# Optimization experiments

Measured on AMD Instinct MI355X. Metric: run time of the kernel, lower is better.

The kernel has to match this reference:

```python
import jax, jax.numpy as jnp
import numpy as np

N = 4096
FEAT = 5
H = 128
L = 3
K = 4
HD = H // K  # 32


def setup_inputs() -> dict:
    key = jax.random.key(0)
    ks = jax.random.split(key, 24)
    node_features = jax.random.normal(ks[0], (N, FEAT), dtype=jnp.float32)
    u = jax.random.uniform(ks[1], (N, N), dtype=jnp.float32)
    adj = jnp.where(u < 0.01, u, 0.0)
    adj = adj / (adj.sum(axis=1, keepdims=True) + 1e-8)  # row-normalised
    mask = jax.random.randint(ks[2], (N,), 0, 2).astype(bool)
    s = 0.05
    return {
        'node_features': node_features,
        'adj': adj,
        'mask': mask,
        'Wi': jax.random.normal(ks[3], (FEAT, H), jnp.float32) * s,
        'bi': jnp.zeros((H,), jnp.float32),
        'gat_W': jax.random.normal(ks[4], (L, K, H, HD), jnp.float32) * s,
        'gat_a': jax.random.normal(ks[5], (L, K, 2 * HD), jnp.float32) * s,
        'ln_g': jnp.ones((L, H), jnp.float32),
        'ln_b': jnp.zeros((L, H), jnp.float32),
        'pW1': jax.random.normal(ks[6], (H, H // 2), jnp.float32) * s,
        'pb1': jnp.zeros((H // 2,), jnp.float32),
        'pW2': jax.random.normal(ks[7], (H // 2, 1), jnp.float32) * s,
        'pb2': jnp.zeros((1,), jnp.float32),
        'poolW': jax.random.normal(ks[8], (H, H), jnp.float32) * s,
        'poolb': jnp.zeros((H,), jnp.float32),
        'poolv': jax.random.normal(ks[9], (H,), jnp.float32) * s,
        'vW1': jax.random.normal(ks[10], (H, H // 2), jnp.float32) * s,
        'vb1': jnp.zeros((H // 2,), jnp.float32),
        'vW2': jax.random.normal(ks[11], (H // 2, 1), jnp.float32) * s,
        'vb2': jnp.zeros((1,), jnp.float32),
    }


def _layernorm(x, g, b, eps=1e-5):
    mu = x.mean(-1, keepdims=True)
    var = ((x - mu) ** 2).mean(-1, keepdims=True)
    return (x - mu) / jnp.sqrt(var + eps) * g + b


def reference(node_features, adj, mask, Wi, bi, gat_W, gat_a, ln_g, ln_b,
              pW1, pb1, pW2, pb2, poolW, poolb, poolv, vW1, vb1, vW2, vb2):
    n = node_features.shape[0]
    x = jax.nn.relu(node_features @ Wi + bi)  # (N, H)
    edge_mask = (adj > 0) | jnp.eye(n, dtype=bool)  # (N, N) incl self-loops
    n_layers = gat_W.shape[0]
    for l in range(n_layers):
        Wx = jnp.einsum('nd,kdh->knh', x, gat_W[l])  # (K, N, hd)
        a_src = jnp.einsum('knh,kh->kn', Wx, gat_a[l][:, :HD])  # (K, N)
        a_dst = jnp.einsum('knh,kh->kn', Wx, gat_a[l][:, HD:])  # (K, N)
        e = jax.nn.leaky_relu(a_src[:, :, None] + a_dst[:, None, :], 0.2)  # (K,N,N)
        e = jnp.where(edge_mask[None], e, -jnp.inf)
        alpha = jax.nn.softmax(e, axis=-1)  # softmax over neighbours j
        h = jax.nn.elu(jnp.einsum('kij,kjh->kih', alpha, Wx))  # (K, N, hd)
        out = jnp.transpose(h, (1, 0, 2)).reshape(n, -1)  # concat heads -> (N, H)
        out = out + x  # residual (Identity: in_dim == out_dim)
        x = _layernorm(out, ln_g[l], ln_b[l])
    # policy head
    logits = (jax.nn.relu(x @ pW1 + pb1) @ pW2 + pb2).squeeze(-1)  # (N,)
    logits = jnp.where(mask, logits, -jnp.inf)
    # attention pooling restricted to masked (valid) nodes
    scores = jnp.tanh(x @ poolW + poolb) @ poolv  # (N,)
    scores = jnp.where(mask, scores, -jnp.inf)
    beta = jax.nn.softmax(scores)
    pooled = (beta[:, None] * x).sum(0)  # (H,)
    value = (jax.nn.relu(pooled @ vW1 + vb1) @ vW2 + vb2).squeeze(-1)  # scalar
    return logits, value
```

## Files before the change

kernel.cpp:

```cpp
#include <hip/hip_runtime.h>

#define NN 4096
#define FEAT 5
#define H 128
#define HD 32
#define KH 4
#define NEG_INF (-__builtin_inff())
#define MASK_SENTINEL (-1e30f)

#define WS_FLAG  0
#define WS_DEG   256
#define WS_NBR   (WS_DEG + NN*4)
#define WS_X     (WS_NBR + NN*128*2)
#define WS_WX    (WS_X + NN*H*4)
#define WS_ATS   (WS_WX + KH*NN*HD*4)
#define WS_ATD   (WS_ATS + NN*16)
#define WS_PART  (WS_ATD + NN*16)
#define WS_ZPART (WS_PART + 256*H*4)

__device__ __forceinline__ float red64(float v) {
#pragma unroll
    for (int off = 32; off; off >>= 1) v += __shfl_xor(v, off, 64);
    return v;
}
__device__ __forceinline__ float red64max(float v) {
#pragma unroll
    for (int off = 32; off; off >>= 1) v = fmaxf(v, __shfl_xor(v, off, 64));
    return v;
}
__device__ __forceinline__ float red32(float v) {
#pragma unroll
    for (int off = 16; off; off >>= 1) v += __shfl_xor(v, off, 32);
    return v;
}
__device__ __forceinline__ bool read_mask(const void* mp, int f, int n) {
    if (f == 3) return ((const long long*)mp)[n] != 0;
    if (f == 1) return ((const int*)mp)[n] != 0;
    if (f == 2) return ((const float*)mp)[n] != 0.f;
    return ((const unsigned char*)mp)[n] != 0;
}

__global__ __launch_bounds__(256) void k_csr_proj(
    const float* __restrict__ adj, const float* __restrict__ nf,
    const float* __restrict__ Wi, const float* __restrict__ bi,
    const void* mask, int* flag, int* __restrict__ deg,
    unsigned short* __restrict__ nbr, float* __restrict__ xbuf) {
    __shared__ int ln[4][128];
    int w = threadIdx.x >> 6, lane = threadIdx.x & 63;
    int row = blockIdx.x * 4 + w;
    ln[w][lane] = 0; ln[w][64 + lane] = 0;
    const float4* arow = (const float4*)(adj + (size_t)row * NN);
    int cnt = 0;
    bool self = false;
    for (int c0 = 0; c0 < NN / 4; c0 += 64) {
        float4 v = arow[c0 + lane];
        int cb = (c0 + lane) * 4;
        float vals[4] = {v.x, v.y, v.z, v.w};
#pragma unroll
        for (int s = 0; s < 4; s++) {
            bool nz = vals[s] > 0.f;
            if (nz && cb + s == row) self = true;
            unsigned long long b = __ballot((int)nz);
            if (nz) {
                int pos = cnt + __popcll(b & ((1ull << lane) - 1ull));
                if (pos < 128) ln[w][pos] = cb + s;
            }
            cnt += __popcll(b);
        }
    }
    bool anyself = __any((int)self);
    if (!anyself) {
        if (lane == 0 && cnt < 128) ln[w][cnt] = row;
        cnt++;
    }
    int d = cnt < 128 ? cnt : 128;
    if (lane == 0) deg[row] = d;
    nbr[(size_t)row * 128 + lane] = (unsigned short)ln[w][lane];
    nbr[(size_t)row * 128 + 64 + lane] = (unsigned short)ln[w][64 + lane];
    float a1 = bi[lane], a2 = bi[64 + lane];
#pragma unroll
    for (int f = 0; f < FEAT; f++) {
        float xv = nf[row * FEAT + f];
        a1 += xv * Wi[f * H + lane];
        a2 += xv * Wi[f * H + 64 + lane];
    }
    xbuf[(size_t)row * H + lane] = fmaxf(a1, 0.f);
    xbuf[(size_t)row * H + 64 + lane] = fmaxf(a2, 0.f);
    if (blockIdx.x == 0 && w == 0) {
        const unsigned* ip = (const unsigned*)mask;
        const float* fp = (const float*)mask;
        bool i32ok = true, i64ok = true, f32ok = true;
        for (int i = lane; i < 1024; i += 64) {
            unsigned v = ip[i];
            if (v > 1u) i32ok = false;
            if (i & 1) { if (v != 0u) i64ok = false; }
            else       { if (v > 1u) i64ok = false; }
            float fv = fp[i];
            if (fv != 0.f && fv != 1.f) f32ok = false;
        }
        i32ok = (__ballot((int)i32ok) == ~0ull);
        i64ok = (__ballot((int)i64ok) == ~0ull);
        f32ok = (__ballot((int)f32ok) == ~0ull);
        if (lane == 0) *flag = i64ok ? 3 : (i32ok ? 1 : (f32ok ? 2 : 0));
    }
}

__global__ __launch_bounds__(256) void k_wx(
    const float* __restrict__ xbuf, const float* __restrict__ gw,
    const float* __restrict__ ga, float* __restrict__ Wx,
    float* __restrict__ attS, float* __restrict__ attD) {
    __shared__ float xs[8][H];
    int t = threadIdx.x;
    int k = t >> 6, lane = t & 63, dh = lane >> 5, h = lane & 31;
    int n0 = blockIdx.x * 8;
    ((float4*)xs)[t] = ((const float4*)(xbuf + (size_t)n0 * H))[t];
    __syncthreads();
    float acc[8] = {0, 0, 0, 0, 0, 0, 0, 0};
    const float* g = gw + (size_t)k * (H * HD) + h;
    for (int dd = 0; dd < 64; dd += 4) {
        int d = dh * 64 + dd;
        float w0 = g[(size_t)(d + 0) * HD];
        float w1 = g[(size_t)(d + 1) * HD];
        float w2 = g[(size_t)(d + 2) * HD];
        float w3 = g[(size_t)(d + 3) * HD];
#pragma unroll
        for (int nn = 0; nn < 8; nn++) {
            float4 xv = *(const float4*)&xs[nn][d];
            acc[nn] += xv.x * w0 + xv.y * w1 + xv.z * w2 + xv.w * w3;
        }
    }
    float aws = ga[k * 64 + h], awd = ga[k * 64 + 32 + h];
#pragma unroll
    for (int nn = 0; nn < 8; nn++) {
        float full = acc[nn] + __shfl_xor(acc[nn], 32, 64);
        float s = red32(full * aws);
        float dv = red32(full * awd);
        int n = n0 + nn;
        if (dh == 0) Wx[(size_t)k * NN * HD + (size_t)n * HD + h] = full;
        if (lane == 0) { attS[n * 4 + k] = s; attD[n * 4 + k] = dv; }
    }
}

__global__ __launch_bounds__(256) void k_agg(
    const int* __restrict__ degG, const unsigned short* __restrict__ nbrG,
    const float* __restrict__ Wx, const float4* __restrict__ attS4,
    const float4* __restrict__ attD4, const float* __restrict__ lng,
    const float* __restrict__ lnb, float* __restrict__ xbuf) {
    __shared__ int s_nbr[128];
    __shared__ float s_o[H];
    __shared__ float s_red[2], s_red2[2];
    int t = threadIdx.x, w = t >> 6, lane = t & 63;
    int node = blockIdx.x;
    int k = w;
    int h = lane & 31, q = lane >> 5;
    int d = degG[node];
    if (t < 128) s_nbr[t] = nbrG[(size_t)node * 128 + t];
    __syncthreads();
    float4 aSv = attS4[node];
    float ai = k == 0 ? aSv.x : k == 1 ? aSv.y : k == 2 ? aSv.z : aSv.w;
    float e0 = NEG_INF, e1 = NEG_INF;
    if (lane < d) {
        float4 dv4 = attD4[s_nbr[lane]];
        float dvv = k == 0 ? dv4.x : k == 1 ? dv4.y : k == 2 ? dv4.z : dv4.w;
        float v = ai + dvv;
        e0 = v > 0.f ? v : 0.2f * v;
    }
    if (64 + lane < d) {
        float4 dv4 = attD4[s_nbr[64 + lane]];
        float dvv = k == 0 ? dv4.x : k == 1 ? dv4.y : k == 2 ? dv4.z : dv4.w;
        float v = ai + dvv;
        e1 = v > 0.f ? v : 0.2f * v;
    }
    float m = red64max(fmaxf(e0, e1));
    float p0 = (lane < d) ? __expf(e0 - m) : 0.f;
    float p1 = (64 + lane < d) ? __expf(e1 - m) : 0.f;
    float inv = 1.f / red64(p0 + p1);
    float acc = 0.f;
    const float* wxk = Wx + (size_t)k * NN * HD + h;
    int jmax = (d + 1) >> 1;
#pragma unroll 4
    for (int j = 0; j < jmax; j++) {
        int c = 2 * j + q;
        int sc = s_nbr[c];
        float al = (c < 64) ? __shfl(p0, c, 64) : __shfl(p1, c - 64, 64);
        acc += al * wxk[(size_t)sc * HD];
    }
    acc += __shfl_xor(acc, 32, 64);
    if (lane < 32) {
        float tot = acc * inv;
        float hv = tot > 0.f ? tot : __expf(tot) - 1.f;
        int dim = k * 32 + h;
        s_o[dim] = hv + xbuf[(size_t)node * H + dim];
    }
    __syncthreads();
    float o = (t < 128) ? s_o[t] : 0.f;
    float ps = red64(o);
    if (lane == 0 && w < 2) s_red[w] = ps;
    __syncthreads();
    float mu = (s_red[0] + s_red[1]) * (1.f / H);
    float dv = o - mu;
    float vs = red64((t < 128) ? dv * dv : 0.f);
    if (lane == 0 && w < 2) s_red2[w] = vs;
    __syncthreads();
    if (t < 128) {
        float var = (s_red2[0] + s_red2[1]) * (1.f / H);
        float rstd = rsqrtf(var + 1e-5f);
        xbuf[(size_t)node * H + t] = dv * rstd * lng[t] + lnb[t];
    }
}

__global__ __launch_bounds__(256) void k_heads(
    const float* __restrict__ xbuf, const float* __restrict__ pW1,
    const float* __restrict__ pb1, const float* __restrict__ pW2,
    const float* __restrict__ pb2, const float* __restrict__ poolW,
    const float* __restrict__ poolb, const float* __restrict__ poolv,
    const void* mask, const int* __restrict__ flag, float* __restrict__ out,
    float* __restrict__ part, float* __restrict__ zpart) {
    __shared__ float lds_x[16][H];
    __shared__ float lds_part[4][H];
    __shared__ float lds_z[4];
    int t = threadIdx.x, w = t >> 6, lane = t & 63;
    int n0b = blockIdx.x * 16;
    for (int idx = t; idx < 16 * H; idx += 256)
        lds_x[idx >> 7][idx & 127] = xbuf[(size_t)(n0b + (idx >> 7)) * H + (idx & 127)];
    __syncthreads();
    int nb = n0b + w * 4;
    float accp[4] = {0, 0, 0, 0}, acs1[4] = {0, 0, 0, 0}, acs2[4] = {0, 0, 0, 0};
#pragma unroll 2
    for (int d = 0; d < H; d++) {
        float w1 = pW1[d * 64 + lane];
        float q1 = poolW[d * H + lane];
        float q2 = poolW[d * H + 64 + lane];
#pragma unroll
        for (int nn = 0; nn < 4; nn++) {
            float xv = lds_x[w * 4 + nn][d];
            accp[nn] += xv * w1;
            acs1[nn] += xv * q1;
            acs2[nn] += xv * q2;
        }
    }
    int flg = *flag;
    float T = fminf(red64(fabsf(poolv[lane]) + fabsf(poolv[64 + lane])), 30.f);
    float pb1v = pb1[lane], pw2v = pW2[lane], pb2v = pb2[0];
    float pob1 = poolb[lane], pob2 = poolb[64 + lane];
    float pov1 = poolv[lane], pov2 = poolv[64 + lane];
    float pp1 = 0.f, pp2 = 0.f, zacc = 0.f;
#pragma unroll
    for (int nn = 0; nn < 4; nn++) {
        int node = nb + nn;
        float hp = red64(fmaxf(accp[nn] + pb1v, 0.f) * pw2v);
        float sc = red64(tanhf(acs1[nn] + pob1) * pov1 + tanhf(acs2[nn] + pob2) * pov2);
        bool mk = read_mask(mask, flg, node);
        if (lane == 0) out[node] = mk ? (hp + pb2v) : MASK_SENTINEL;
        float wn = mk ? __expf(sc - T) : 0.f;
        pp1 += wn * lds_x[w * 4 + nn][lane];
        pp2 += wn * lds_x[w * 4 + nn][64 + lane];
        zacc += wn;
    }
    lds_part[w][lane] = pp1;
    lds_part[w][64 + lane] = pp2;
    if (lane == 0) lds_z[w] = zacc;
    __syncthreads();
    if (w == 0) {
        float s1 = lds_part[0][lane] + lds_part[1][lane] + lds_part[2][lane] + lds_part[3][lane];
        float s2 = lds_part[0][64 + lane] + lds_part[1][64 + lane] +
                   lds_part[2][64 + lane] + lds_part[3][64 + lane];
        part[blockIdx.x * H + lane] = s1;
        part[blockIdx.x * H + 64 + lane] = s2;
        if (lane == 0) zpart[blockIdx.x] = lds_z[0] + lds_z[1] + lds_z[2] + lds_z[3];
    }
}

__global__ __launch_bounds__(1024) void k_value(
    const float* __restrict__ part, const float* __restrict__ zpart,
    const float* __restrict__ vW1, const float* __restrict__ vb1,
    const float* __restrict__ vW2, const float* __restrict__ vb2,
    float* __restrict__ out) {
    __shared__ float segsum[8][H];
    __shared__ float zfin[256];
    __shared__ float pooled[H];
    int t = threadIdx.x;
    int dim = t & 127, seg = t >> 7;
    float s = 0.f;
#pragma unroll 8
    for (int b = seg * 32; b < seg * 32 + 32; b++) s += part[b * H + dim];
    segsum[seg][dim] = s;
    if (t < 256) zfin[t] = zpart[t];
    __syncthreads();
    if (t < 512) {
        int sg = t >> 7;
        segsum[sg][dim] += segsum[sg + 4][dim];
    }
    if (t >= 512 && t < 640) zfin[t - 512] += zfin[t - 512 + 128];
    __syncthreads();
    if (t < 256) {
        int sg = t >> 7;
        segsum[sg][dim] += segsum[sg + 2][dim];
    }
    if (t >= 512 && t < 576) zfin[t - 512] += zfin[t - 512 + 64];
    __syncthreads();
    if (t < 128) segsum[0][dim] += segsum[1][dim];
    if (t >= 512 && t < 544) zfin[t - 512] += zfin[t - 512 + 32];
    __syncthreads();
    if (t < 32) {
        float z = zfin[t];
#pragma unroll
        for (int off = 16; off; off >>= 1) z += __shfl_xor(z, off, 32);
        if (t == 0) zfin[0] = z;
    }
    __syncthreads();
    float Z = zfin[0];
    if (t < H) pooled[t] = segsum[0][t] / Z;
    __syncthreads();
    if (t < 64) {
        float acc = vb1[t];
#pragma unroll 4
        for (int d = 0; d < H; d++) acc += pooled[d] * vW1[d * 64 + t];
        float v = red64(fmaxf(acc, 0.f) * vW2[t]);
        if (t == 0) out[NN] = v + vb2[0];
    }
}

extern "C" void kernel_launch(void* const* d_in, const int* in_sizes, int n_in,
                              void* d_out, int out_size, void* d_ws, size_t ws_size,
                              hipStream_t stream) {
    const float* nf    = (const float*)d_in[0];
    const float* adj   = (const float*)d_in[1];
    const void*  mask  = d_in[2];
    const float* Wi    = (const float*)d_in[3];
    const float* bi    = (const float*)d_in[4];
    const float* gat_W = (const float*)d_in[5];
    const float* gat_a = (const float*)d_in[6];
    const float* ln_g  = (const float*)d_in[7];
    const float* ln_b  = (const float*)d_in[8];
    const float* pW1   = (const float*)d_in[9];
    const float* pb1   = (const float*)d_in[10];
    const float* pW2   = (const float*)d_in[11];
    const float* pb2   = (const float*)d_in[12];
    const float* poolW = (const float*)d_in[13];
    const float* poolb = (const float*)d_in[14];
    const float* poolv = (const float*)d_in[15];
    const float* vW1   = (const float*)d_in[16];
    const float* vb1   = (const float*)d_in[17];
    const float* vW2   = (const float*)d_in[18];
    const float* vb2   = (const float*)d_in[19];

    char* ws = (char*)d_ws;
    int*            flag = (int*)(ws + WS_FLAG);
    int*            deg  = (int*)(ws + WS_DEG);
    unsigned short* nbr  = (unsigned short*)(ws + WS_NBR);
    float* xbuf  = (float*)(ws + WS_X);
    float* Wx    = (float*)(ws + WS_WX);
    float* ats   = (float*)(ws + WS_ATS);
    float* atd   = (float*)(ws + WS_ATD);
    float* partb = (float*)(ws + WS_PART);
    float* zpart = (float*)(ws + WS_ZPART);
    float* out   = (float*)d_out;

    const size_t GWL = KH * H * HD;
    const size_t GAL = KH * 2 * HD;

    k_csr_proj<<<1024, 256, 0, stream>>>(adj, nf, Wi, bi, mask, flag, deg, nbr, xbuf);
    for (int l = 0; l < 3; l++) {
        k_wx<<<512, 256, 0, stream>>>(xbuf, gat_W + l * GWL, gat_a + l * GAL,
                                      Wx, ats, atd);
        k_agg<<<4096, 256, 0, stream>>>(deg, nbr, Wx, (const float4*)ats,
                                        (const float4*)atd, ln_g + l * H,
                                        ln_b + l * H, xbuf);
    }
    k_heads<<<256, 256, 0, stream>>>(xbuf, pW1, pb1, pW2, pb2, poolW, poolb, poolv,
                                     mask, flag, out, partb, zpart);
    k_value<<<1, 1024, 0, stream>>>(partb, zpart, vW1, vb1, vW2, vb2, out);
}
```

Baseline: 178.0 us.

## Store Wx node-major and aggregate one node per wavefront with all heads

Wx is now written node-major (N x 128) instead of head-major, so each neighbour's four-head feature row is one contiguous 512-byte segment. k_agg now processes four nodes per block, one wavefront each. Each wave computes the softmax for all four heads at once and stores the normalised alphas in shared memory. Each lane then gathers float2 features and does the ELU, residual and layernorm with wave reductions only, which removes the block-wide barriers and shared-memory layernorm. The cost is more registers per lane and unconditional loads for padded neighbour slots, which depends on the neighbour padding holding valid indices.

```diff
diff --git a/kernel.cpp b/kernel.cpp
--- a/kernel.cpp
+++ b/kernel.cpp
@@ -13,7 +13,7 @@
 #define WS_NBR   (WS_DEG + NN*4)
 #define WS_X     (WS_NBR + NN*128*2)
 #define WS_WX    (WS_X + NN*H*4)
-#define WS_ATS   (WS_WX + KH*NN*HD*4)
+#define WS_ATS   (WS_WX + NN*H*4)
 #define WS_ATD   (WS_ATS + NN*16)
 #define WS_PART  (WS_ATD + NN*16)
 #define WS_ZPART (WS_PART + 256*H*4)
@@ -136,77 +136,81 @@
         float s = red32(full * aws);
         float dv = red32(full * awd);
         int n = n0 + nn;
-        if (dh == 0) Wx[(size_t)k * NN * HD + (size_t)n * HD + h] = full;
+        if (dh == 0) Wx[(size_t)n * H + k * 32 + h] = full;
         if (lane == 0) { attS[n * 4 + k] = s; attD[n * 4 + k] = dv; }
     }
 }
 
 __global__ __launch_bounds__(256) void k_agg(
     const int* __restrict__ degG, const unsigned short* __restrict__ nbrG,
-    const float* __restrict__ Wx, const float4* __restrict__ attS4,
+    const float* __restrict__ Wxn, const float4* __restrict__ attS4,
     const float4* __restrict__ attD4, const float* __restrict__ lng,
     const float* __restrict__ lnb, float* __restrict__ xbuf) {
-    __shared__ int s_nbr[128];
-    __shared__ float s_o[H];
-    __shared__ float s_red[2], s_red2[2];
+    __shared__ int s_nbr[4][128];
+    __shared__ float s_al[4][128][4];
     int t = threadIdx.x, w = t >> 6, lane = t & 63;
-    int node = blockIdx.x;
-    int k = w;
-    int h = lane & 31, q = lane >> 5;
+    int node = blockIdx.x * 4 + w;
     int d = degG[node];
-    if (t < 128) s_nbr[t] = nbrG[(size_t)node * 128 + t];
-    __syncthreads();
-    float4 aSv = attS4[node];
-    float ai = k == 0 ? aSv.x : k == 1 ? aSv.y : k == 2 ? aSv.z : aSv.w;
-    float e0 = NEG_INF, e1 = NEG_INF;
-    if (lane < d) {
-        float4 dv4 = attD4[s_nbr[lane]];
-        float dvv = k == 0 ? dv4.x : k == 1 ? dv4.y : k == 2 ? dv4.z : dv4.w;
-        float v = ai + dvv;
-        e0 = v > 0.f ? v : 0.2f * v;
-    }
-    if (64 + lane < d) {
-        float4 dv4 = attD4[s_nbr[64 + lane]];
-        float dvv = k == 0 ? dv4.x : k == 1 ? dv4.y : k == 2 ? dv4.z : dv4.w;
-        float v = ai + dvv;
-        e1 = v > 0.f ? v : 0.2f * v;
-    }
-    float m = red64max(fmaxf(e0, e1));
-    float p0 = (lane < d) ? __expf(e0 - m) : 0.f;
-    float p1 = (64 + lane < d) ? __expf(e1 - m) : 0.f;
-    float inv = 1.f / red64(p0 + p1);
-    float acc = 0.f;
-    const float* wxk = Wx + (size_t)k * NN * HD + h;
-    int jmax = (d + 1) >> 1;
-#pragma unroll 4
-    for (int j = 0; j < jmax; j++) {
-        int c = 2 * j + q;
-        int sc = s_nbr[c];
-        float al = (c < 64) ? __shfl(p0, c, 64) : __shfl(p1, c - 64, 64);
-        acc += al * wxk[(size_t)sc * HD];
-    }
-    acc += __shfl_xor(acc, 32, 64);
-    if (lane < 32) {
-        float tot = acc * inv;
-        float hv = tot > 0.f ? tot : __expf(tot) - 1.f;
-        int dim = k * 32 + h;
-        s_o[dim] = hv + xbuf[(size_t)node * H + dim];
-    }
-    __syncthreads();
-    float o = (t < 128) ? s_o[t] : 0.f;
-    float ps = red64(o);
-    if (lane == 0 && w < 2) s_red[w] = ps;
-    __syncthreads();
-    float mu = (s_red[0] + s_red[1]) * (1.f / H);
-    float dv = o - mu;
-    float vs = red64((t < 128) ? dv * dv : 0.f);
-    if (lane == 0 && w < 2) s_red2[w] = vs;
-    __syncthreads();
-    if (t < 128) {
-        float var = (s_red2[0] + s_red2[1]) * (1.f / H);
-        float rstd = rsqrtf(var + 1e-5f);
-        xbuf[(size_t)node * H + t] = dv * rstd * lng[t] + lnb[t];
-    }
+    const unsigned short* np = nbrG + (size_t)node * 128;
+    int sn0 = np[lane], sn1 = np[64 + lane];
+    s_nbr[w][lane] = sn0;
+    s_nbr[w][64 + lane] = sn1;
+    float4 aS = attS4[node];
+    float4 d0 = attD4[sn0], d1 = attD4[sn1];
+    bool v0 = lane < d, v1 = 64 + lane < d;
+#define LRELU(x) ((x) > 0.f ? (x) : 0.2f * (x))
+    float e0x = v0 ? LRELU(aS.x + d0.x) : NEG_INF;
+    float e0y = v0 ? LRELU(aS.y + d0.y) : NEG_INF;
+    float e0z = v0 ? LRELU(aS.z + d0.z) : NEG_INF;
+    float e0w = v0 ? LRELU(aS.w + d0.w) : NEG_INF;
+    float e1x = v1 ? LRELU(aS.x + d1.x) : NEG_INF;
+    float e1y = v1 ? LRELU(aS.y + d1.y) : NEG_INF;
+    float e1z = v1 ? LRELU(aS.z + d1.z) : NEG_INF;
+    float e1w = v1 ? LRELU(aS.w + d1.w) : NEG_INF;
+#undef LRELU
+    float mx = red64max(fmaxf(e0x, e1x));
+    float my = red64max(fmaxf(e0y, e1y));
+    float mz = red64max(fmaxf(e0z, e1z));
+    float mw = red64max(fmaxf(e0w, e1w));
+    float p0x = v0 ? __expf(e0x - mx) : 0.f, p1x = v1 ? __expf(e1x - mx) : 0.f;
+    float p0y = v0 ? __expf(e0y - my) : 0.f, p1y = v1 ? __expf(e1y - my) : 0.f;
+    float p0z = v0 ? __expf(e0z - mz) : 0.f, p1z = v1 ? __expf(e1z - mz) : 0.f;
+    float p0w = v0 ? __expf(e0w - mw) : 0.f, p1w = v1 ? __expf(e1w - mw) : 0.f;
+    float ix = 1.f / red64(p0x + p1x);
+    float iy = 1.f / red64(p0y + p1y);
+    float iz = 1.f / red64(p0z + p1z);
+    float iw = 1.f / red64(p0w + p1w);
+    float4 a0 = make_float4(p0x * ix, p0y * iy, p0z * iz, p0w * iw);
+    float4 a1 = make_float4(p1x * ix, p1y * iy, p1z * iz, p1w * iw);
+    *(float4*)&s_al[w][lane][0] = a0;
+    *(float4*)&s_al[w][64 + lane][0] = a1;
+    int ksel = lane >> 4;
+    int dim0 = 2 * lane;
+    float acc0 = 0.f, acc1 = 0.f;
+    int dpad = (d + 7) & ~7;
+    for (int c0 = 0; c0 < dpad; c0 += 8) {
+#pragma unroll
+        for (int j = 0; j < 8; j++) {
+            int c = c0 + j;
+            int sc = s_nbr[w][c];
+            float al = s_al[w][c][ksel];
+            float2 v = *(const float2*)(Wxn + (size_t)sc * H + dim0);
+            acc0 += al * v.x;
+            acc1 += al * v.y;
+        }
+    }
+    float2 xr = *(const float2*)(xbuf + (size_t)node * H + dim0);
+    float h0 = acc0 > 0.f ? acc0 : __expf(acc0) - 1.f;
+    float h1 = acc1 > 0.f ? acc1 : __expf(acc1) - 1.f;
+    float o0 = h0 + xr.x, o1 = h1 + xr.y;
+    float mu = red64(o0 + o1) * (1.f / H);
+    float dv0 = o0 - mu, dv1 = o1 - mu;
+    float var = red64(dv0 * dv0 + dv1 * dv1) * (1.f / H);
+    float rstd = rsqrtf(var + 1e-5f);
+    float2 ov;
+    ov.x = dv0 * rstd * lng[dim0] + lnb[dim0];
+    ov.y = dv1 * rstd * lng[dim0 + 1] + lnb[dim0 + 1];
+    *(float2*)(xbuf + (size_t)node * H + dim0) = ov;
 }
 
 __global__ __launch_bounds__(256) void k_heads(
@@ -364,7 +368,7 @@
     for (int l = 0; l < 3; l++) {
         k_wx<<<512, 256, 0, stream>>>(xbuf, gat_W + l * GWL, gat_a + l * GAL,
                                       Wx, ats, atd);
-        k_agg<<<4096, 256, 0, stream>>>(deg, nbr, Wx, (const float4*)ats,
+        k_agg<<<1024, 256, 0, stream>>>(deg, nbr, Wx, (const float4*)ats,
                                         (const float4*)atd, ln_g + l * H,
                                         ln_b + l * H, xbuf);
     }
```

Measured after the change: 146.2 us. -17.9%, faster.
